# Kernel tuning notes

Hardware: AMD Instinct MI355X
Metric: run time of the kernel (lower is better)

Reference implementation:

```python
import jax, jax.numpy as jnp
import numpy as np

N_E = 16384
E_DIM = 256
SRC_DIM = 1024
BETA = 0.25


def setup_inputs() -> dict:
    key = jax.random.key(0)
    k_x, k_ew, k_eb, k_cb, k_dw, k_db = jax.random.split(key, 6)
    x = jax.random.normal(k_x, (16, 576, SRC_DIM), dtype=jnp.float32)
    # encoder Linear(source_dim -> embed_dim)
    enc_w = jax.random.normal(k_ew, (SRC_DIM, E_DIM), dtype=jnp.float32) / np.sqrt(SRC_DIM)
    enc_b = jax.random.normal(k_eb, (E_DIM,), dtype=jnp.float32) * 0.01
    # codebook initialized uniform(-1/n_e, 1/n_e) as in the torch module
    codebook = jax.random.uniform(k_cb, (N_E, E_DIM), dtype=jnp.float32, minval=-1.0 / N_E, maxval=1.0 / N_E)
    # decoder Linear(embed_dim -> source_dim)
    dec_w = jax.random.normal(k_dw, (E_DIM, SRC_DIM), dtype=jnp.float32) / np.sqrt(E_DIM)
    dec_b = jax.random.normal(k_db, (SRC_DIM,), dtype=jnp.float32) * 0.01
    return {"x": x, "enc_w": enc_w, "enc_b": enc_b, "codebook": codebook, "dec_w": dec_w, "dec_b": dec_b}


def reference(x, enc_w, enc_b, codebook, dec_w, dec_b):
    # encode: [B,S,src] -> [B,S,e]
    z = jnp.einsum('bsd,de->bse', x, enc_w) + enc_b
    # squared distances to all codebook entries: ||z||^2 + ||E||^2 - 2 z.E^T
    z2 = jnp.sum(z * z, axis=-1, keepdims=True)            # [B,S,1]
    e2 = jnp.sum(codebook * codebook, axis=-1)             # [n_e]
    cross = jnp.einsum('bse,ne->bsn', z, codebook)         # [B,S,n_e]
    d = z2 + e2 - 2.0 * cross
    idx = jnp.argmin(d, axis=-1)                           # [B,S] int
    z_q = codebook[idx]                                    # [B,S,e]
    sg = jax.lax.stop_gradient
    loss = BETA * jnp.mean((sg(z_q) - z) ** 2) + jnp.mean((z_q - sg(z)) ** 2)
    z_q_st = z + sg(z_q - z)                               # straight-through
    out = jnp.einsum('bse,ed->bsd', z_q_st, dec_w) + dec_b
    return (out, loss)
```

## Files before the change

kernel.cpp:

```cpp
#include <hip/hip_runtime.h>

typedef __bf16 bf16;
typedef __bf16 bf16x8 __attribute__((ext_vector_type(8)));
typedef float f32x4 __attribute__((ext_vector_type(4)));
typedef int i32x8 __attribute__((ext_vector_type(8)));
typedef unsigned int u32;
typedef unsigned char u8;

#define N_TOK 9216
#define SRC 1024
#define EDIM 256
#define NE 16384
#define GROUPS 16
#define GSIZE 1024
#define NBLK_LOSS 144
#define NEG_CB_SCALE -8192.0f
#define E2_SCALE 4096.0f
#define LOSS_DENOM 2359296.0f

__device__ __forceinline__ void async_load16(const void* g, void* l) {
  __builtin_amdgcn_global_load_lds(
      (__attribute__((address_space(1))) void*)(void*)(const_cast<void*>(g)),
      (__attribute__((address_space(3))) void*)l, 16, 0, 0);
}

__device__ __forceinline__ f32x4 mfma16(bf16x8 a, bf16x8 b, f32x4 c) {
  return __builtin_amdgcn_mfma_f32_16x16x32_bf16(a, b, c, 0, 0, 0);
}
__device__ __forceinline__ f32x4 mfma_mx(i32x8 a, i32x8 b, f32x4 c) {
  return __builtin_amdgcn_mfma_scale_f32_16x16x128_f8f6f4(
      a, b, c, 0, 0, 0, 0x7F7F7F7F, 0, 0x7F7F7F7F);
}

__global__ __launch_bounds__(256) void k_prep(const float* __restrict__ enc_w,
                                              const float* __restrict__ dec_w,
                                              const float* __restrict__ cb,
                                              bf16* __restrict__ enc_wT,
                                              bf16* __restrict__ dec_wT,
                                              u32* __restrict__ cbb8,
                                              float* __restrict__ e2s) {
  int b = blockIdx.x;
  if (b < 128) {
    __shared__ float T[64][65];
    const float* In;
    bf16* Out;
    int R, C, ti, tj;
    if (b < 64) {
      In = enc_w; Out = enc_wT; R = 1024; C = 256;
      ti = b & 15; tj = b >> 4;
    } else {
      int t2 = b - 64;
      In = dec_w; Out = dec_wT; R = 256; C = 1024;
      ti = t2 & 3; tj = t2 >> 2;
    }
    int c0 = threadIdx.x & 63, r0 = threadIdx.x >> 6;
#pragma unroll
    for (int i = 0; i < 16; i++) {
      int rr = r0 + i * 4;
      T[rr][c0] = In[(size_t)(ti * 64 + rr) * C + tj * 64 + c0];
    }
    __syncthreads();
#pragma unroll
    for (int i = 0; i < 16; i++) {
      int rr = r0 + i * 4;
      Out[(size_t)(tj * 64 + rr) * R + ti * 64 + c0] = (bf16)T[c0][rr];
    }
  } else {
    int row = (b - 128) * 4 + (threadIdx.x >> 6);
    int lane = threadIdx.x & 63;
    int slot = lane >> 2;
    int h = (slot & 8) | ((slot & 7) ^ (row & 7));
    int k0 = h * 16 + (lane & 3) * 4;
    float4 v = *(const float4*)(cb + (size_t)row * EDIM + k0);
    int pk = __builtin_amdgcn_cvt_pk_fp8_f32(v.x * NEG_CB_SCALE, v.y * NEG_CB_SCALE, 0, false);
    pk = __builtin_amdgcn_cvt_pk_fp8_f32(v.z * NEG_CB_SCALE, v.w * NEG_CB_SCALE, pk, true);
    cbb8[(size_t)row * 64 + lane] = (u32)pk;
    float sq = v.x * v.x + v.y * v.y + v.z * v.z + v.w * v.w;
#pragma unroll
    for (int off = 32; off; off >>= 1) sq += __shfl_xor(sq, off, 64);
    if (lane == 0) e2s[row] = E2_SCALE * (sq + 1.0f);
  }
}

__global__ __launch_bounds__(256) void k_enc(const float* __restrict__ x,
                                             const bf16* __restrict__ wT,
                                             const float* __restrict__ bias,
                                             u8* __restrict__ z8) {
  __shared__ __align__(16) bf16 As[2][64 * 32];
  __shared__ __align__(16) bf16 Bs[2][64 * 32];
  const int tid = threadIdx.x;
  const int wid = tid >> 6, lane = tid & 63;
  const int col = lane & 15, quad = lane >> 4;
  const int wm = (wid >> 1) * 32, wn = (wid & 1) * 32;
  const int bm = blockIdx.x * 64, bn = blockIdx.y * 64;
  f32x4 acc[2][2] = {};
  const int arow = tid >> 2, ags = tid & 3;

  float4 q0, q1;
  auto loadA = [&](int kc) {
    const float* p = x + (size_t)(bm + arow) * SRC + kc + ags * 8;
    q0 = *(const float4*)p;
    q1 = *(const float4*)(p + 4);
  };
  auto writeA = [&](int bb) {
    bf16x8 o = {(bf16)q0.x, (bf16)q0.y, (bf16)q0.z, (bf16)q0.w,
                (bf16)q1.x, (bf16)q1.y, (bf16)q1.z, (bf16)q1.w};
    *(bf16x8*)((char*)&As[bb][0] + (arow * 4 + (ags ^ (arow & 3))) * 16) = o;
  };
  auto stageB = [&](int kc, int bb) {
    int row = tid >> 2;
    int gg = (tid & 3) ^ (row & 3);
    async_load16(wT + (size_t)(bn + row) * SRC + kc + gg * 8,
                 (char*)&Bs[bb][0] + wid * 1024);
  };

  loadA(0);
  writeA(0);
  stageB(0, 0);
  for (int it = 0; it < 32; it++) {
    int cbuf = it & 1, nbuf = cbuf ^ 1;
    __syncthreads();
    if (it < 31) {
      loadA((it + 1) * 32);
      stageB((it + 1) * 32, nbuf);
    }
    bf16x8 afr[2], bfr[2];
#pragma unroll
    for (int t = 0; t < 2; t++) {
      int row = wm + t * 16 + col;
      afr[t] = *(const bf16x8*)((const char*)&As[cbuf][0] +
                                (row * 4 + (quad ^ (row & 3))) * 16);
    }
#pragma unroll
    for (int u = 0; u < 2; u++) {
      int row = wn + u * 16 + col;
      bfr[u] = *(const bf16x8*)((const char*)&Bs[cbuf][0] +
                                (row * 4 + (quad ^ (row & 3))) * 16);
    }
#pragma unroll
    for (int t = 0; t < 2; t++)
#pragma unroll
      for (int u = 0; u < 2; u++) acc[t][u] = mfma16(afr[t], bfr[u], acc[t][u]);
    if (it < 31) writeA(nbuf);
  }
#pragma unroll
  for (int u = 0; u < 2; u++) {
    int n = bn + wn + u * 16 + col;
    float bv = bias[n];
#pragma unroll
    for (int t = 0; t < 2; t++)
#pragma unroll
      for (int r = 0; r < 4; r++) {
        int m = bm + wm + t * 16 + quad * 4 + r;
        float v = acc[t][u][r] + bv;
        int pk = __builtin_amdgcn_cvt_pk_fp8_f32(v, v, 0, false);
        z8[(size_t)m * EDIM + n] = (u8)(pk & 0xFF);
      }
  }
}

__global__ __launch_bounds__(256, 3) void k_argmin(const u8* __restrict__ zb8,
                                                   const u8* __restrict__ cbb8,
                                                   const float* __restrict__ e2s,
                                                   float* __restrict__ pval,
                                                   int* __restrict__ pidx) {
  __shared__ __align__(16) u8 Cs[2 * 16384];
  __shared__ __align__(16) float Es[1024];
  const int tid = threadIdx.x;
  const int wid = tid >> 6, lane = tid & 63;
  const int col = lane & 15, quad = lane >> 4;
  const int g = blockIdx.y;
  const int tw = blockIdx.x * 192 + wid * 48;

  async_load16((const u8*)(e2s + g * GSIZE) + (size_t)tid * 16,
               (char*)Es + wid * 1024);

  i32x8 af[3][2];
#pragma unroll
  for (int t = 0; t < 3; t++)
#pragma unroll
    for (int m = 0; m < 2; m++) {
      const u8* p = zb8 + (size_t)(tw + t * 16 + col) * EDIM + m * 128 + quad * 32;
      int4 lo = *(const int4*)p;
      int4 hi = *(const int4*)(p + 16);
      af[t][m] = (i32x8){lo.x, lo.y, lo.z, lo.w, hi.x, hi.y, hi.z, hi.w};
    }

  u32 best[3][4];
#pragma unroll
  for (int t = 0; t < 3; t++)
#pragma unroll
    for (int r = 0; r < 4; r++) best[t][r] = 0xFFFFFFFFu;

  auto stage_load = [&](int st, int bb) {
    const u8* src = cbb8 + (size_t)(g * GSIZE + st * 64) * EDIM;
#pragma unroll
    for (int j = 0; j < 4; j++) {
      async_load16(src + (wid * 256 + j * 64 + lane) * 16,
                   (char*)Cs + bb * 16384 + wid * 4096 + j * 1024);
    }
  };

  auto compute = [&](int st, int bb) {
    const char* bbase = (const char*)Cs + bb * 16384;
    float ev[4];
#pragma unroll
    for (int u = 0; u < 4; u++) ev[u] = Es[st * 64 + u * 16 + col];
    f32x4 c[3][4];
#pragma unroll
    for (int t = 0; t < 3; t++)
#pragma unroll
      for (int u = 0; u < 4; u++)
        c[t][u] = (f32x4){ev[u], ev[u], ev[u], ev[u]};
    const int r7 = col & 7;
#pragma unroll
    for (int m = 0; m < 2; m++) {
#pragma unroll
      for (int u = 0; u < 4; u++) {
        int row = u * 16 + col;
        int s0 = m * 8 + ((2 * quad) ^ r7);
        int s1 = m * 8 + ((2 * quad + 1) ^ r7);
        int4 b0 = *(const int4*)(bbase + row * 256 + s0 * 16);
        int4 b1 = *(const int4*)(bbase + row * 256 + s1 * 16);
        i32x8 bfr = (i32x8){b0.x, b0.y, b0.z, b0.w, b1.x, b1.y, b1.z, b1.w};
#pragma unroll
        for (int t = 0; t < 3; t++) c[t][u] = mfma_mx(af[t][m], bfr, c[t][u]);
      }
    }
#pragma unroll
    for (int t = 0; t < 3; t++)
#pragma unroll
      for (int r = 0; r < 4; r++) {
        u32 k0 = (__float_as_uint(c[t][0][r]) & 0xFFFFFFC0u) | (u32)(st * 4 + 0);
        u32 k1 = (__float_as_uint(c[t][1][r]) & 0xFFFFFFC0u) | (u32)(st * 4 + 1);
        u32 k2 = (__float_as_uint(c[t][2][r]) & 0xFFFFFFC0u) | (u32)(st * 4 + 2);
        u32 k3 = (__float_as_uint(c[t][3][r]) & 0xFFFFFFC0u) | (u32)(st * 4 + 3);
        u32 a = k0 < k1 ? k0 : k1;
        u32 bm_ = k2 < k3 ? k2 : k3;
        u32 m_ = a < bm_ ? a : bm_;
        best[t][r] = m_ < best[t][r] ? m_ : best[t][r];
      }
  };

  stage_load(0, 0);
  for (int st = 0; st < 16; st++) {
    __syncthreads();
    if (st < 15) stage_load(st + 1, (st + 1) & 1);
    compute(st, st & 1);
  }

#pragma unroll
  for (int t = 0; t < 3; t++)
#pragma unroll
    for (int r = 0; r < 4; r++) {
      u32 key = best[t][r];
      int cw = col;
#pragma unroll
      for (int off = 1; off < 16; off <<= 1) {
        u32 ok = (u32)__shfl_xor((int)key, off, 64);
        int oc = __shfl_xor(cw, off, 64);
        if (ok < key) { key = ok; cw = oc; }
      }
      if (col == 0) {
        int token = tw + t * 16 + quad * 4 + r;
        pval[token * GROUPS + g] = __uint_as_float(key & 0xFFFFFFC0u);
        pidx[token * GROUPS + g] = g * GSIZE + (int)(key & 63u) * 16 + cw;
      }
    }
}

__global__ __launch_bounds__(256) void k_dec(const float* __restrict__ cb,
                                             const float* __restrict__ pval,
                                             const int* __restrict__ pidx,
                                             const u8* __restrict__ zb8,
                                             const bf16* __restrict__ wT,
                                             const float* __restrict__ bias,
                                             float* __restrict__ out,
                                             float* __restrict__ lpart) {
  __shared__ __align__(16) bf16 As[2][64 * 32];
  __shared__ __align__(16) bf16 Bs[2][256 * 32];
  __shared__ int idxL[64];
  __shared__ float lsred[4];
  const int tid = threadIdx.x;
  const int wid = tid >> 6, lane = tid & 63;
  const int col = lane & 15, quad = lane >> 4;
  const int wm = (wid >> 1) * 32, wn = (wid & 1) * 128;
  const int bm = blockIdx.x * 64, bn = blockIdx.y * 256;
  const bool do_loss = (blockIdx.y == 0);

  {
    int tl = tid >> 2, j0 = tid & 3;
    float v = 3.4e38f;
    int idx = 0;
#pragma unroll
    for (int jj = 0; jj < 4; jj++) {
      int grp = j0 * 4 + jj;
      float ov = pval[(bm + tl) * GROUPS + grp];
      int oi = pidx[(bm + tl) * GROUPS + grp];
      if (ov < v || (ov == v && oi < idx)) { v = ov; idx = oi; }
    }
#pragma unroll
    for (int off = 1; off < 4; off <<= 1) {
      float ov = __shfl_xor(v, off, 64);
      int oi = __shfl_xor(idx, off, 64);
      if (ov < v || (ov == v && oi < idx)) { v = ov; idx = oi; }
    }
    if (j0 == 0) idxL[tl] = idx;
  }
  __syncthreads();

  const int arow = tid >> 2, ags = tid & 3;
  const int ridx = idxL[arow];
  float lacc = 0.f;
  f32x4 acc[2][8] = {};

  float4 q0, q1;
  auto loadA = [&](int kc) {
    const float* p = cb + (size_t)ridx * EDIM + kc + ags * 8;
    q0 = *(const float4*)p;
    q1 = *(const float4*)(p + 4);
    if (do_loss) {
      u32 zw0 = *(const u32*)(zb8 + (size_t)(bm + arow) * EDIM + kc + ags * 8);
      u32 zw1 = *(const u32*)(zb8 + (size_t)(bm + arow) * EDIM + kc + ags * 8 + 4);
      float d0 = q0.x - __builtin_amdgcn_cvt_f32_fp8(zw0, 0);
      float d1 = q0.y - __builtin_amdgcn_cvt_f32_fp8(zw0, 1);
      float d2 = q0.z - __builtin_amdgcn_cvt_f32_fp8(zw0, 2);
      float d3 = q0.w - __builtin_amdgcn_cvt_f32_fp8(zw0, 3);
      float d4 = q1.x - __builtin_amdgcn_cvt_f32_fp8(zw1, 0);
      float d5 = q1.y - __builtin_amdgcn_cvt_f32_fp8(zw1, 1);
      float d6 = q1.z - __builtin_amdgcn_cvt_f32_fp8(zw1, 2);
      float d7 = q1.w - __builtin_amdgcn_cvt_f32_fp8(zw1, 3);
      lacc += d0 * d0 + d1 * d1 + d2 * d2 + d3 * d3 +
              d4 * d4 + d5 * d5 + d6 * d6 + d7 * d7;
    }
  };
  auto writeA = [&](int bb) {
    bf16x8 o = {(bf16)q0.x, (bf16)q0.y, (bf16)q0.z, (bf16)q0.w,
                (bf16)q1.x, (bf16)q1.y, (bf16)q1.z, (bf16)q1.w};
    *(bf16x8*)((char*)&As[bb][0] + (arow * 4 + (ags ^ (arow & 3))) * 16) = o;
  };
  auto stageB = [&](int kc, int bb) {
#pragma unroll
    for (int j = 0; j < 4; j++) {
      int slot = wid * 256 + j * 64 + lane;
      int row = slot >> 2;
      int gg = (slot & 3) ^ (row & 3);
      async_load16(wT + (size_t)(bn + row) * EDIM + kc + gg * 8,
                   (char*)&Bs[bb][0] + wid * 4096 + j * 1024);
    }
  };

  loadA(0);
  writeA(0);
  stageB(0, 0);
  for (int it = 0; it < 8; it++) {
    int cbuf = it & 1, nbuf = cbuf ^ 1;
    __syncthreads();
    if (it < 7) {
      loadA((it + 1) * 32);
      stageB((it + 1) * 32, nbuf);
    }
    bf16x8 afr[2], bfr[8];
#pragma unroll
    for (int t = 0; t < 2; t++) {
      int row = wm + t * 16 + col;
      afr[t] = *(const bf16x8*)((const char*)&As[cbuf][0] +
                                (row * 4 + (quad ^ (row & 3))) * 16);
    }
#pragma unroll
    for (int u = 0; u < 8; u++) {
      int row = wn + u * 16 + col;
      bfr[u] = *(const bf16x8*)((const char*)&Bs[cbuf][0] +
                                (row * 4 + (quad ^ (row & 3))) * 16);
    }
#pragma unroll
    for (int t = 0; t < 2; t++)
#pragma unroll
      for (int u = 0; u < 8; u++) acc[t][u] = mfma16(afr[t], bfr[u], acc[t][u]);
    if (it < 7) writeA(nbuf);
  }

#pragma unroll
  for (int u = 0; u < 8; u++) {
    int n = bn + wn + u * 16 + col;
    float bv = bias[n];
#pragma unroll
    for (int t = 0; t < 2; t++)
#pragma unroll
      for (int r = 0; r < 4; r++) {
        int m = bm + wm + t * 16 + quad * 4 + r;
        out[(size_t)m * SRC + n] = acc[t][u][r] + bv;
      }
  }

  if (do_loss) {
#pragma unroll
    for (int off = 32; off; off >>= 1) lacc += __shfl_xor(lacc, off, 64);
    if (lane == 0) lsred[wid] = lacc;
    __syncthreads();
    if (tid == 0) lpart[blockIdx.x] = lsred[0] + lsred[1] + lsred[2] + lsred[3];
  }
}

__global__ __launch_bounds__(256) void k_loss(const float* __restrict__ lpart,
                                              float* __restrict__ outl) {
  float s = 0.f;
  if (threadIdx.x < NBLK_LOSS) s = lpart[threadIdx.x];
#pragma unroll
  for (int off = 32; off; off >>= 1) s += __shfl_xor(s, off, 64);
  __shared__ float ls[4];
  int wv = threadIdx.x >> 6;
  if ((threadIdx.x & 63) == 0) ls[wv] = s;
  __syncthreads();
  if (threadIdx.x == 0) *outl = 1.25f * (ls[0] + ls[1] + ls[2] + ls[3]) / LOSS_DENOM;
}

extern "C" void kernel_launch(void* const* d_in, const int* in_sizes, int n_in,
                              void* d_out, int out_size, void* d_ws, size_t ws_size,
                              hipStream_t stream) {
  const float* x = (const float*)d_in[0];
  const float* enc_w = (const float*)d_in[1];
  const float* enc_b = (const float*)d_in[2];
  const float* cb = (const float*)d_in[3];
  const float* dec_w = (const float*)d_in[4];
  const float* dec_b = (const float*)d_in[5];
  float* out = (float*)d_out;
  float* out_loss = out + (size_t)N_TOK * SRC;

  char* ws = (char*)d_ws;
  bf16* enc_wT = (bf16*)(ws + 0);
  bf16* dec_wT = (bf16*)(ws + 524288);
  u8* zb8 = (u8*)(ws + 1048576);
  u32* cbb8 = (u32*)(ws + 3407872);
  float* e2s = (float*)(ws + 7602176);
  float* pval = (float*)(ws + 7667712);
  int* pidx = (int*)(ws + 8257536);
  float* lpart = (float*)(ws + 8847360);

  k_prep<<<4224, 256, 0, stream>>>(enc_w, dec_w, cb, enc_wT, dec_wT, cbb8, e2s);
  k_enc<<<dim3(144, 4), 256, 0, stream>>>(x, enc_wT, enc_b, zb8);
  k_argmin<<<dim3(48, GROUPS), 256, 0, stream>>>(zb8, (const u8*)cbb8, e2s, pval, pidx);
  k_dec<<<dim3(144, 4), 256, 0, stream>>>(cb, pval, pidx, zb8, dec_wT, dec_b, out, lpart);
  k_loss<<<1, 256, 0, stream>>>(lpart, out_loss);
}
```

Measured before the change: 188.9 us.

## Interleave codebook LDS reads with MFMA per sub-tile using fine-grained barriers and priority

Restructures the distance/argmin main loop so each 16-row codebook sub-tile is read from LDS, multiplied with MFMA and reduced before moving to the next. The next stage's async global-to-LDS load is issued partway through the current stage. Explicit s_barrier/s_waitcnt, sched_barrier and s_setprio are added to interleave LDS traffic with MFMA across waves and to cut register pressure from holding 12 accumulators. The extra barriers per sub-tile add synchronization overhead and depend on the manual waitcnt placement being correct.

New measurement: 186.9 us. Within noise of the previous version (-1.1%).

```diff
diff --git a/kernel.cpp b/kernel.cpp
--- a/kernel.cpp
+++ b/kernel.cpp
@@ -201,52 +201,53 @@
     }
   };
 
-  auto compute = [&](int st, int bb) {
-    const char* bbase = (const char*)Cs + bb * 16384;
-    float ev[4];
-#pragma unroll
-    for (int u = 0; u < 4; u++) ev[u] = Es[st * 64 + u * 16 + col];
-    f32x4 c[3][4];
-#pragma unroll
-    for (int t = 0; t < 3; t++)
-#pragma unroll
-      for (int u = 0; u < 4; u++)
-        c[t][u] = (f32x4){ev[u], ev[u], ev[u], ev[u]};
-    const int r7 = col & 7;
-#pragma unroll
-    for (int m = 0; m < 2; m++) {
-#pragma unroll
-      for (int u = 0; u < 4; u++) {
-        int row = u * 16 + col;
-        int s0 = m * 8 + ((2 * quad) ^ r7);
-        int s1 = m * 8 + ((2 * quad + 1) ^ r7);
-        int4 b0 = *(const int4*)(bbase + row * 256 + s0 * 16);
-        int4 b1 = *(const int4*)(bbase + row * 256 + s1 * 16);
-        i32x8 bfr = (i32x8){b0.x, b0.y, b0.z, b0.w, b1.x, b1.y, b1.z, b1.w};
-#pragma unroll
-        for (int t = 0; t < 3; t++) c[t][u] = mfma_mx(af[t][m], bfr, c[t][u]);
+  stage_load(0, 0);
+  asm volatile("s_waitcnt vmcnt(0)" ::: "memory");
+  __builtin_amdgcn_s_barrier();
+
+  const int r7 = col & 7;
+  const int s0 = ((2 * quad) ^ r7) * 16;
+  const int s1 = ((2 * quad + 1) ^ r7) * 16;
+
+  for (int st = 0; st < 16; st++) {
+    const char* bbase = (const char*)Cs + (st & 1) * 16384;
+#pragma unroll
+    for (int u = 0; u < 4; u++) {
+      const int rb = (u * 16 + col) * 256;
+      int4 a0 = *(const int4*)(bbase + rb + s0);
+      int4 a1 = *(const int4*)(bbase + rb + s1);
+      int4 b0 = *(const int4*)(bbase + rb + 128 + s0);
+      int4 b1 = *(const int4*)(bbase + rb + 128 + s1);
+      float ev = Es[st * 64 + u * 16 + col];
+      if (u == 1 && st < 15) stage_load(st + 1, (st & 1) ^ 1);
+      __builtin_amdgcn_s_barrier();
+      asm volatile("s_waitcnt lgkmcnt(0)" ::: "memory");
+      __builtin_amdgcn_sched_barrier(0);
+      __builtin_amdgcn_s_setprio(1);
+      i32x8 bm0 = (i32x8){a0.x, a0.y, a0.z, a0.w, a1.x, a1.y, a1.z, a1.w};
+      i32x8 bm1 = (i32x8){b0.x, b0.y, b0.z, b0.w, b1.x, b1.y, b1.z, b1.w};
+      f32x4 c0 = (f32x4){ev, ev, ev, ev};
+      f32x4 c1 = c0, c2 = c0;
+      c0 = mfma_mx(af[0][0], bm0, c0);
+      c1 = mfma_mx(af[1][0], bm0, c1);
+      c2 = mfma_mx(af[2][0], bm0, c2);
+      c0 = mfma_mx(af[0][1], bm1, c0);
+      c1 = mfma_mx(af[1][1], bm1, c1);
+      c2 = mfma_mx(af[2][1], bm1, c2);
+      __builtin_amdgcn_s_setprio(0);
+      const u32 code = (u32)(st * 4 + u);
+#pragma unroll
+      for (int r = 0; r < 4; r++) {
+        u32 k0 = (__float_as_uint(c0[r]) & 0xFFFFFFC0u) | code;
+        u32 k1 = (__float_as_uint(c1[r]) & 0xFFFFFFC0u) | code;
+        u32 k2 = (__float_as_uint(c2[r]) & 0xFFFFFFC0u) | code;
+        best[0][r] = k0 < best[0][r] ? k0 : best[0][r];
+        best[1][r] = k1 < best[1][r] ? k1 : best[1][r];
+        best[2][r] = k2 < best[2][r] ? k2 : best[2][r];
       }
     }
-#pragma unroll
-    for (int t = 0; t < 3; t++)
-#pragma unroll
-      for (int r = 0; r < 4; r++) {
-        u32 k0 = (__float_as_uint(c[t][0][r]) & 0xFFFFFFC0u) | (u32)(st * 4 + 0);
-        u32 k1 = (__float_as_uint(c[t][1][r]) & 0xFFFFFFC0u) | (u32)(st * 4 + 1);
-        u32 k2 = (__float_as_uint(c[t][2][r]) & 0xFFFFFFC0u) | (u32)(st * 4 + 2);
-        u32 k3 = (__float_as_uint(c[t][3][r]) & 0xFFFFFFC0u) | (u32)(st * 4 + 3);
-        u32 a = k0 < k1 ? k0 : k1;
-        u32 bm_ = k2 < k3 ? k2 : k3;
-        u32 m_ = a < bm_ ? a : bm_;
-        best[t][r] = m_ < best[t][r] ? m_ : best[t][r];
-      }
-  };
-
-  stage_load(0, 0);
-  for (int st = 0; st < 16; st++) {
-    __syncthreads();
-    if (st < 15) stage_load(st + 1, (st + 1) & 1);
-    compute(st, st & 1);
+    if (st < 15) asm volatile("s_waitcnt vmcnt(0)" ::: "memory");
+    __builtin_amdgcn_s_barrier();
   }
 
 #pragma unroll
```
